# Performance work log

Hardware: AMD Instinct MI355X
Metric: run time of the kernel (lower is better)

## Reference

```python
import jax, jax.numpy as jnp
import numpy as np

N = 50000      # nodes
E = 800000     # edges
G = 1024       # graphs in batch
D_IN = 9       # atom feature dim
D = 64         # embedding_size


def _lin(k, fan_in, shape):
    s = 1.0 / np.sqrt(fan_in)
    return jax.random.uniform(k, shape, jnp.float32, -s, s)


def setup_inputs() -> dict:
    key = jax.random.key(0)
    ks = jax.random.split(key, 12)
    x = jax.random.normal(ks[0], (N, D_IN), dtype=jnp.float32)
    edge_index = jax.random.randint(ks[1], (2, E), 0, N, dtype=jnp.int32)
    # node -> graph id, sorted, every graph non-empty
    batch = (jnp.arange(N) * G // N).astype(jnp.int32)
    W0 = _lin(ks[2], D_IN, (D_IN, D)); b0 = _lin(ks[3], D_IN, (D,))
    W1 = _lin(ks[4], D, (D, D));       b1 = _lin(ks[5], D, (D,))
    W2 = _lin(ks[6], D, (D, D));       b2 = _lin(ks[7], D, (D,))
    W3 = _lin(ks[8], D, (D, D));       b3 = _lin(ks[9], D, (D,))
    Wout = _lin(ks[10], 2 * D, (2 * D, 1)); bout = _lin(ks[11], 2 * D, (1,))
    return {"x": x, "edge_index": edge_index, "batch": batch,
            "W0": W0, "b0": b0, "W1": W1, "b1": b1,
            "W2": W2, "b2": b2, "W3": W3, "b3": b3,
            "Wout": Wout, "bout": bout}


def reference(x, edge_index, batch, W0, b0, W1, b1, W2, b2, W3, b3, Wout, bout):
    n = x.shape[0]
    # GCNConv: add self-loops, symmetric normalization D^-1/2 (A+I) D^-1/2
    loops = jnp.arange(n, dtype=edge_index.dtype)
    row = jnp.concatenate([edge_index[0], loops])  # source
    col = jnp.concatenate([edge_index[1], loops])  # destination
    deg = jax.ops.segment_sum(jnp.ones_like(col, dtype=x.dtype), col, num_segments=n)
    dinv = jax.lax.rsqrt(deg)  # deg >= 1 thanks to self-loops
    norm = dinv[row] * dinv[col]  # [E+N]

    def conv(h, W, b):
        h = h @ W                               # [N, D]
        msg = norm[:, None] * h[row]            # [E+N, D]
        return jax.ops.segment_sum(msg, col, num_segments=n) + b

    h = jnp.tanh(conv(x, W0, b0))
    h = jnp.tanh(conv(h, W1, b1))
    h = jnp.tanh(conv(h, W2, b2))
    h = jnp.tanh(conv(h, W3, b3))
    # dropout is identity in eval mode
    gmax = jax.ops.segment_max(h, batch, num_segments=G)                       # [G, D]
    cnt = jax.ops.segment_sum(jnp.ones((n, 1), h.dtype), batch, num_segments=G)
    gmean = jax.ops.segment_sum(h, batch, num_segments=G) / jnp.maximum(cnt, 1.0)
    pooled = jnp.concatenate([gmax, gmean], axis=1)                            # [G, 2D]
    return pooled @ Wout + bout
```

## Files before the change

kernel.cpp:

```cpp
#include <hip/hip_runtime.h>
#include <hip/hip_fp16.h>
#include <math.h>

#define N_NODES 50000
#define N_EDGES 800000
#define N_GRAPHS 1024
#define DIM 64
#define PAD 64
#define ZROW N_NODES

#define BSHIFT 8
#define BDEST 256
#define NB 196
#define CAP_B 6144
#define EPB 4096

typedef int   v4i __attribute__((ext_vector_type(4)));
typedef float v4f __attribute__((ext_vector_type(4)));

__device__ __forceinline__ int4 ntld4i(const int* p) {
    v4i v = __builtin_nontemporal_load((const v4i*)p);
    return make_int4(v[0], v[1], v[2], v[3]);
}


__global__ void fill_p1(const int* __restrict__ row, const int* __restrict__ col,
                        int* __restrict__ bcnt, unsigned* __restrict__ bbuf) {
    __shared__ int hist[NB];
    __shared__ int base[NB];
    int tid = threadIdx.x;
    if (tid < NB) hist[tid] = 0;
    __syncthreads();

    int e0 = blockIdx.x * EPB;
    int bk[16]; int rk[16]; unsigned pk[16];
#pragma unroll
    for (int i = 0; i < 4; ++i) {
        int e4 = e0 + i * 1024 + tid * 4;
        bool ok = e4 < N_EDGES;
        int4 c = ok ? ntld4i(col + e4) : make_int4(0, 0, 0, 0);
        int4 r = ok ? ntld4i(row + e4) : make_int4(0, 0, 0, 0);
        int cc[4] = {c.x, c.y, c.z, c.w};
        int rr[4] = {r.x, r.y, r.z, r.w};
#pragma unroll
        for (int j = 0; j < 4; ++j) {
            int q = i * 4 + j;
            if (ok) {
                bk[q] = cc[j] >> BSHIFT;
                pk[q] = ((unsigned)rr[j] << BSHIFT) | (unsigned)(cc[j] & (BDEST - 1));
                rk[q] = atomicAdd(&hist[bk[q]], 1);
            } else {
                bk[q] = -1; rk[q] = 0; pk[q] = 0;
            }
        }
    }
    __syncthreads();
    if (tid < NB) base[tid] = atomicAdd(&bcnt[tid], hist[tid]);
    __syncthreads();
#pragma unroll
    for (int q = 0; q < 16; ++q) {
        if (bk[q] >= 0) {
            int pos = base[bk[q]] + rk[q];
            if (pos < CAP_B) bbuf[(size_t)bk[q] * CAP_B + pos] = pk[q];
        }
    }
}


__global__ void fill_p2(const int* __restrict__ bcnt, const unsigned* __restrict__ bbuf,
                        int* __restrict__ ideg, unsigned short* __restrict__ esrc) {
    __shared__ unsigned short srow[BDEST * PAD];
    __shared__ int ldeg[BDEST];
    int tid = threadIdx.x;
    int b = blockIdx.x;
    {
        uint4* s4 = (uint4*)srow;
        for (int i = tid; i < BDEST * PAD / 8; i += 256) s4[i] = make_uint4(0, 0, 0, 0);
        ldeg[tid] = 0;
    }
    __syncthreads();

    int cnt = min(bcnt[b], CAP_B);
    const unsigned* bp = bbuf + (size_t)b * CAP_B;
    for (int e = tid; e < cnt; e += 256) {
        unsigned u = bp[e];
        int local = u & (BDEST - 1);
        int src = (int)(u >> BSHIFT);
        int k = atomicAdd(&ldeg[local], 1);
        if (k < PAD) srow[local * PAD + k] = (unsigned short)src;
    }
    __syncthreads();

    int dest0 = b << BSHIFT;
    {
        int node = dest0 + tid;
        if (node < N_NODES) ideg[node] = ldeg[tid];
    }
    const uint4* s4 = (const uint4*)srow;
#pragma unroll
    for (int i = 0; i < 8; ++i) {
        int idx = tid + 256 * i;
        int local = idx >> 3;
        int node = dest0 + local;
        if (node < N_NODES)
            ((uint4*)(esrc + (size_t)node * PAD))[idx & 7] = s4[idx];
    }
}


__global__ void gemm9(const float* __restrict__ x, const float* __restrict__ W,
                      const int* __restrict__ ideg, __half* __restrict__ th) {
    __shared__ float Wl[9 * DIM];
    int tid = threadIdx.x;
    if (blockIdx.x == 0 && tid < DIM) th[(size_t)ZROW * DIM + tid] = __float2half(0.0f);
    for (int i = tid; i < 9 * DIM; i += 256) Wl[i] = W[i];
    __syncthreads();
    int node = blockIdx.x * 4 + (tid >> 6);
    int d = tid & 63;
    if (node >= N_NODES) return;
    const float* xr = x + (size_t)node * 9;
    float acc = 0.0f;
#pragma unroll
    for (int k = 0; k < 9; ++k) acc += xr[k] * Wl[k * DIM + d];
    float dv = rsqrtf((float)ideg[node] + 1.0f);
    th[(size_t)node * DIM + d] = __float2half(dv * acc);
}

__global__ void gemm64(const float* __restrict__ h, const float* __restrict__ W,
                       const int* __restrict__ ideg, uint2* __restrict__ th2) {
    __shared__ float At[64][68];
    __shared__ float Bl[64][68];
    int tid = threadIdx.x;
    int n0 = blockIdx.x * 64;

    {
        const float4* W4 = (const float4*)W;
#pragma unroll
        for (int i = 0; i < 4; ++i) {
            int idx = tid + 256 * i;
            int k = idx >> 4;
            int d4 = idx & 15;
            float4 v = W4[idx];
            *(float4*)&Bl[k][d4 * 4] = v;
        }
    }
    {
        int node = tid >> 2;
        int seg = tid & 3;
        int gn = n0 + node;
        bool ok = gn < N_NODES;
        const float4* h4 = (const float4*)h;
#pragma unroll
        for (int i = 0; i < 4; ++i) {
            int c4 = seg * 4 + i;
            float4 v = ok ? h4[(size_t)gn * 16 + c4] : make_float4(0.f, 0.f, 0.f, 0.f);
            int d = c4 * 4;
            At[d + 0][node] = v.x;
            At[d + 1][node] = v.y;
            At[d + 2][node] = v.z;
            At[d + 3][node] = v.w;
        }
    }
    __syncthreads();

    int ty = tid >> 4;
    int tx = tid & 15;
    float c00 = 0, c01 = 0, c02 = 0, c03 = 0;
    float c10 = 0, c11 = 0, c12 = 0, c13 = 0;
    float c20 = 0, c21 = 0, c22 = 0, c23 = 0;
    float c30 = 0, c31 = 0, c32 = 0, c33 = 0;
#pragma unroll 8
    for (int k = 0; k < 64; ++k) {
        float4 a = *(const float4*)&At[k][ty * 4];
        float4 b = *(const float4*)&Bl[k][tx * 4];
        c00 += a.x * b.x; c01 += a.x * b.y; c02 += a.x * b.z; c03 += a.x * b.w;
        c10 += a.y * b.x; c11 += a.y * b.y; c12 += a.y * b.z; c13 += a.y * b.w;
        c20 += a.z * b.x; c21 += a.z * b.y; c22 += a.z * b.z; c23 += a.z * b.w;
        c30 += a.w * b.x; c31 += a.w * b.y; c32 += a.w * b.z; c33 += a.w * b.w;
    }
    int gn = n0 + ty * 4;
#define STORE_ROW(r, CA, CB, CC, CD)                                          \
    if (gn + r < N_NODES) {                                                   \
        float dv = rsqrtf((float)ideg[gn + r] + 1.0f);                        \
        __half2 p0 = __floats2half2_rn(dv * CA, dv * CB);                     \
        __half2 p1 = __floats2half2_rn(dv * CC, dv * CD);                     \
        uint2 o;                                                              \
        o.x = *(unsigned*)&p0;                                                \
        o.y = *(unsigned*)&p1;                                                \
        th2[(size_t)(gn + r) * 16 + tx] = o;                                  \
    }
    STORE_ROW(0, c00, c01, c02, c03)
    STORE_ROW(1, c10, c11, c12, c13)
    STORE_ROW(2, c20, c21, c22, c23)
    STORE_ROW(3, c30, c31, c32, c33)
#undef STORE_ROW
}


__device__ __forceinline__ float4 h4tof4(uint2 v) {
    __half2 a = *reinterpret_cast<const __half2*>(&v.x);
    __half2 c = *reinterpret_cast<const __half2*>(&v.y);
    float2 fa = __half22float2(a);
    float2 fc = __half22float2(c);
    return make_float4(fa.x, fa.y, fc.x, fc.y);
}

__device__ __forceinline__ void add4(float4& a, const float4& r) {
    a.x += r.x; a.y += r.y; a.z += r.z; a.w += r.w;
}

__global__ __launch_bounds__(256, 6)
void gather_tanh(const unsigned short* __restrict__ esrc, const int* __restrict__ ideg,
                 const uint2* __restrict__ th2, const float* __restrict__ b,
                 float4* __restrict__ hout4) {
    int tid = threadIdx.x;
    int wid = tid >> 6;
    int lane = tid & 63;
    int sub = lane & 15;
    int grp = lane >> 4;
    int node = blockIdx.x * 16 + wid * 4 + grp;

    int deg = min(ideg[node], PAD);
    const uint4* ep4 = (const uint4*)(esrc + node * PAD);
    const uint2* tb = th2 + sub;

    float4 acc0 = h4tof4(tb[(size_t)node * 16]);
    float4 acc1 = make_float4(0.f, 0.f, 0.f, 0.f);
    float4 acc2 = make_float4(0.f, 0.f, 0.f, 0.f);
    float4 acc3 = make_float4(0.f, 0.f, 0.f, 0.f);

    for (int base = 0; base < deg; base += 8) {
        uint4 u = ep4[base >> 3];
        unsigned w[4] = {u.x, u.y, u.z, u.w};
        int idx[8];
#pragma unroll
        for (int j = 0; j < 4; ++j) {
            idx[2 * j + 0] = (int)(w[j] & 0xffffu);
            idx[2 * j + 1] = (int)(w[j] >> 16);
        }
        int rem = deg - base;
        uint2 r[8];
#pragma unroll
        for (int j = 0; j < 8; ++j) {
            int s = (j < rem) ? idx[j] : ZROW;
            r[j] = tb[(size_t)s * 16];
        }
#pragma unroll
        for (int j = 0; j < 8; ++j) {
            float4 v = h4tof4(r[j]);
            if ((j & 3) == 0) add4(acc0, v);
            else if ((j & 3) == 1) add4(acc1, v);
            else if ((j & 3) == 2) add4(acc2, v);
            else add4(acc3, v);
        }
    }

    float4 acc;
    acc.x = (acc0.x + acc1.x) + (acc2.x + acc3.x);
    acc.y = (acc0.y + acc1.y) + (acc2.y + acc3.y);
    acc.z = (acc0.z + acc1.z) + (acc2.z + acc3.z);
    acc.w = (acc0.w + acc1.w) + (acc2.w + acc3.w);

    float4 bv = ((const float4*)b)[sub];
    float dv = rsqrtf((float)deg + 1.0f);
    float4 res;
    res.x = tanhf(dv * acc.x + bv.x);
    res.y = tanhf(dv * acc.y + bv.y);
    res.z = tanhf(dv * acc.z + bv.z);
    res.w = tanhf(dv * acc.w + bv.w);
    hout4[(size_t)node * 16 + sub] = res;
}


__device__ __forceinline__ int lower_bound(const int* a, int n, int key) {
    int lo = 0, hi = n;
    while (lo < hi) {
        int mid = (lo + hi) >> 1;
        if (a[mid] < key) lo = mid + 1; else hi = mid;
    }
    return lo;
}

__global__ void pool_out(const float* __restrict__ h, const int* __restrict__ batch,
                         const float* __restrict__ Wout, const float* __restrict__ bout,
                         float* __restrict__ out) {
    __shared__ float smax[4][DIM];
    __shared__ float ssum[4][DIM];
    __shared__ int bounds[2];
    int g = blockIdx.x;
    int tid = threadIdx.x, w = tid >> 6, d = tid & 63;
    if (tid == 0) {
        bounds[0] = lower_bound(batch, N_NODES, g);
        bounds[1] = lower_bound(batch, N_NODES, g + 1);
    }
    __syncthreads();
    int start = bounds[0], end = bounds[1];
    float mx = -INFINITY, sum = 0.0f;
    for (int n = start + w; n < end; n += 4) {
        float v = h[(size_t)n * DIM + d];
        mx = fmaxf(mx, v);
        sum += v;
    }
    smax[w][d] = mx;
    ssum[w][d] = sum;
    __syncthreads();
    if (w == 0) {
        mx = fmaxf(fmaxf(smax[0][d], smax[1][d]), fmaxf(smax[2][d], smax[3][d]));
        sum = ssum[0][d] + ssum[1][d] + ssum[2][d] + ssum[3][d];
        float cnt = (float)(end - start);
        float mean = sum / fmaxf(cnt, 1.0f);
        float v = mx * Wout[d] + mean * Wout[DIM + d];
#pragma unroll
        for (int off = 32; off > 0; off >>= 1) v += __shfl_down(v, off, 64);
        if (d == 0) out[g] = v + bout[0];
    }
}


static inline size_t align256(size_t x) { return (x + 255) & ~(size_t)255; }

extern "C" void kernel_launch(void* const* d_in, const int* in_sizes, int n_in,
                              void* d_out, int out_size, void* d_ws, size_t ws_size,
                              hipStream_t stream) {
    const float* x     = (const float*)d_in[0];
    const int*   ei    = (const int*)d_in[1];
    const int*   batch = (const int*)d_in[2];
    const float* W0    = (const float*)d_in[3];
    const float* b0    = (const float*)d_in[4];
    const float* W1    = (const float*)d_in[5];
    const float* b1    = (const float*)d_in[6];
    const float* W2    = (const float*)d_in[7];
    const float* b2    = (const float*)d_in[8];
    const float* W3    = (const float*)d_in[9];
    const float* b3    = (const float*)d_in[10];
    const float* Wout  = (const float*)d_in[11];
    const float* bout  = (const float*)d_in[12];
    float* out = (float*)d_out;

    const int* row = ei;
    const int* col = ei + N_EDGES;

    char* ws = (char*)d_ws;
    size_t off = 0;
    int*            ideg = (int*)(ws + off);            off += align256((size_t)N_NODES * 4);
    unsigned short* esrc = (unsigned short*)(ws + off); off += align256((size_t)N_NODES * PAD * 2);
    __half*         th   = (__half*)(ws + off);         off += align256(((size_t)N_NODES + 1) * DIM * 2);
    float*          hA   = (float*)(ws + off);          off += align256((size_t)N_NODES * DIM * 4);
    unsigned*       bbuf = (unsigned*)(ws + off);       off += align256((size_t)NB * CAP_B * 4);
    int*            bcnt = (int*)(ws + off);            off += align256((size_t)NB * 4);
    (void)ws_size;

    const int wave_blocks = N_NODES / 4;
    const int gath_blocks = N_NODES / 16;
    const int gemm_blocks = (N_NODES + 63) / 64;

    hipMemsetAsync(bcnt, 0, (size_t)NB * 4, stream);
    fill_p1<<<NB, 256, 0, stream>>>(row, col, bcnt, bbuf);
    fill_p2<<<NB, 256, 0, stream>>>(bcnt, bbuf, ideg, esrc);

    gemm9<<<wave_blocks, 256, 0, stream>>>(x, W0, ideg, th);
    gather_tanh<<<gath_blocks, 256, 0, stream>>>(esrc, ideg, (const uint2*)th, b0, (float4*)hA);

    const float* Ws[3] = {W1, W2, W3};
    const float* bs[3] = {b1, b2, b3};
    for (int l = 0; l < 3; ++l) {
        gemm64<<<gemm_blocks, 256, 0, stream>>>(hA, Ws[l], ideg, (uint2*)th);
        gather_tanh<<<gath_blocks, 256, 0, stream>>>(esrc, ideg, (const uint2*)th, bs[l], (float4*)hA);
    }

    pool_out<<<N_GRAPHS, 256, 0, stream>>>(hA, batch, Wout, bout, out);
    (void)out_size; (void)n_in; (void)in_sizes;
}
```

Before: 239.2 us.

## Sort nodes by in-degree so gather waves process balanced neighbor counts

Adds a counting-sort pass (histogram, prefix, scatter) that builds a permutation of nodes grouped by clamped in-degree. The four gather layers then read node and degree from this permutation, so the four node groups sharing a wave have similar loop trip counts and diverge less. The gather kernel also drops from four to two accumulators and raises the launch-bounds occupancy hint from 6 to 8. The cost is three small extra kernels per call and scattered, non-sequential output writes; the degree clamp moves from 64 to 63, which could drop one neighbor for nodes of degree 64 or more.

```diff
diff --git a/kernel.cpp b/kernel.cpp
--- a/kernel.cpp
+++ b/kernel.cpp
@@ -105,6 +105,34 @@
         if (node < N_NODES)
             ((uint4*)(esrc + (size_t)node * PAD))[idx & 7] = s4[idx];
     }
+}
+
+
+__global__ void bin_hist(const int* __restrict__ ideg, int* __restrict__ dhist) {
+    __shared__ int h[64];
+    int tid = threadIdx.x;
+    if (tid < 64) h[tid] = 0;
+    __syncthreads();
+    int n = blockIdx.x * 256 + tid;
+    if (n < N_NODES) atomicAdd(&h[min(ideg[n], 63)], 1);
+    __syncthreads();
+    if (tid < 64 && h[tid]) atomicAdd(&dhist[tid], h[tid]);
+}
+
+__global__ void bin_prefix(const int* __restrict__ dhist, int* __restrict__ dbase) {
+    if (threadIdx.x == 0) {
+        int acc = 0;
+        for (int i = 0; i < 64; ++i) { dbase[i] = acc; acc += dhist[i]; }
+    }
+}
+
+__global__ void bin_scatter(const int* __restrict__ ideg, int* __restrict__ dbase,
+                            unsigned* __restrict__ perm) {
+    int n = blockIdx.x * 256 + threadIdx.x;
+    if (n >= N_NODES) return;
+    int d = min(ideg[n], 63);
+    int pos = atomicAdd(&dbase[d], 1);
+    perm[pos] = ((unsigned)d << 16) | (unsigned)n;
 }
 
 
@@ -209,8 +237,8 @@
     a.x += r.x; a.y += r.y; a.z += r.z; a.w += r.w;
 }
 
-__global__ __launch_bounds__(256, 6)
-void gather_tanh(const unsigned short* __restrict__ esrc, const int* __restrict__ ideg,
+__global__ __launch_bounds__(256, 8)
+void gather_tanh(const unsigned short* __restrict__ esrc, const unsigned* __restrict__ perm,
                  const uint2* __restrict__ th2, const float* __restrict__ b,
                  float4* __restrict__ hout4) {
     int tid = threadIdx.x;
@@ -218,16 +246,16 @@
     int lane = tid & 63;
     int sub = lane & 15;
     int grp = lane >> 4;
-    int node = blockIdx.x * 16 + wid * 4 + grp;
-
-    int deg = min(ideg[node], PAD);
+    int slot = blockIdx.x * 16 + wid * 4 + grp;
+    unsigned pw = perm[slot];
+    int node = (int)(pw & 0xffffu);
+    int deg = (int)(pw >> 16);
+
     const uint4* ep4 = (const uint4*)(esrc + node * PAD);
     const uint2* tb = th2 + sub;
 
     float4 acc0 = h4tof4(tb[(size_t)node * 16]);
     float4 acc1 = make_float4(0.f, 0.f, 0.f, 0.f);
-    float4 acc2 = make_float4(0.f, 0.f, 0.f, 0.f);
-    float4 acc3 = make_float4(0.f, 0.f, 0.f, 0.f);
 
     for (int base = 0; base < deg; base += 8) {
         uint4 u = ep4[base >> 3];
@@ -248,18 +276,16 @@
 #pragma unroll
         for (int j = 0; j < 8; ++j) {
             float4 v = h4tof4(r[j]);
-            if ((j & 3) == 0) add4(acc0, v);
-            else if ((j & 3) == 1) add4(acc1, v);
-            else if ((j & 3) == 2) add4(acc2, v);
-            else add4(acc3, v);
+            if ((j & 1) == 0) add4(acc0, v);
+            else              add4(acc1, v);
         }
     }
 
     float4 acc;
-    acc.x = (acc0.x + acc1.x) + (acc2.x + acc3.x);
-    acc.y = (acc0.y + acc1.y) + (acc2.y + acc3.y);
-    acc.z = (acc0.z + acc1.z) + (acc2.z + acc3.z);
-    acc.w = (acc0.w + acc1.w) + (acc2.w + acc3.w);
+    acc.x = acc0.x + acc1.x;
+    acc.y = acc0.y + acc1.y;
+    acc.z = acc0.z + acc1.z;
+    acc.w = acc0.w + acc1.w;
 
     float4 bv = ((const float4*)b)[sub];
     float dv = rsqrtf((float)deg + 1.0f);
@@ -348,24 +374,32 @@
     float*          hA   = (float*)(ws + off);          off += align256((size_t)N_NODES * DIM * 4);
     unsigned*       bbuf = (unsigned*)(ws + off);       off += align256((size_t)NB * CAP_B * 4);
     int*            bcnt = (int*)(ws + off);            off += align256((size_t)NB * 4);
+    int*            dhist= (int*)(ws + off);            off += align256(64 * 4);
+    int*            dbase= (int*)(ws + off);            off += align256(64 * 4);
+    unsigned*       perm = (unsigned*)(ws + off);       off += align256((size_t)N_NODES * 4);
     (void)ws_size;
 
+    const int node_blocks = (N_NODES + 255) / 256;
     const int wave_blocks = N_NODES / 4;
     const int gath_blocks = N_NODES / 16;
     const int gemm_blocks = (N_NODES + 63) / 64;
 
     hipMemsetAsync(bcnt, 0, (size_t)NB * 4, stream);
+    hipMemsetAsync(dhist, 0, 64 * 4, stream);
     fill_p1<<<NB, 256, 0, stream>>>(row, col, bcnt, bbuf);
     fill_p2<<<NB, 256, 0, stream>>>(bcnt, bbuf, ideg, esrc);
+    bin_hist<<<node_blocks, 256, 0, stream>>>(ideg, dhist);
+    bin_prefix<<<1, 64, 0, stream>>>(dhist, dbase);
+    bin_scatter<<<node_blocks, 256, 0, stream>>>(ideg, dbase, perm);
 
     gemm9<<<wave_blocks, 256, 0, stream>>>(x, W0, ideg, th);
-    gather_tanh<<<gath_blocks, 256, 0, stream>>>(esrc, ideg, (const uint2*)th, b0, (float4*)hA);
+    gather_tanh<<<gath_blocks, 256, 0, stream>>>(esrc, perm, (const uint2*)th, b0, (float4*)hA);
 
     const float* Ws[3] = {W1, W2, W3};
     const float* bs[3] = {b1, b2, b3};
     for (int l = 0; l < 3; ++l) {
         gemm64<<<gemm_blocks, 256, 0, stream>>>(hA, Ws[l], ideg, (uint2*)th);
-        gather_tanh<<<gath_blocks, 256, 0, stream>>>(esrc, ideg, (const uint2*)th, bs[l], (float4*)hA);
+        gather_tanh<<<gath_blocks, 256, 0, stream>>>(esrc, perm, (const uint2*)th, bs[l], (float4*)hA);
     }
 
     pool_out<<<N_GRAPHS, 256, 0, stream>>>(hA, batch, Wout, bout, out);
```

Measured after the change: 378.8 us. +58.4%, slower.
